# Kernel optimization log

Measured on AMD Instinct MI355X. Metric: run time of the kernel, lower is better.

Reference implementation:

```python
import jax, jax.numpy as jnp
import numpy as np

B, F, C, NS, P, N = 256, 2048, 16384, 65536, 8, 32
T, W_BU, W_H, P_MARGIN, N_MARGIN = 1.0, 1.0, 10.0, 0.1, 0.1


def setup_inputs() -> dict:
    key = jax.random.key(0)
    ks = jax.random.split(key, 8)
    inputs = jax.random.normal(ks[0], (B, F), jnp.float32)
    targets = jax.random.randint(ks[1], (B,), 0, C)
    # batch global indices: unique (original .item() assumes a single match)
    indexs = jax.random.permutation(ks[2], NS)[:B].astype(jnp.int64) if False else jax.random.permutation(ks[2], jnp.arange(NS))[:B]
    # positive candidates drawn from in-batch indices so they are found in `indexs`
    pos_sel = jax.random.randint(ks[3], (B, P), 0, B)
    ppairs = indexs[pos_sel]
    # negative candidates: arbitrary global indices (mostly not in batch)
    npairs = jax.random.randint(ks[4], (B, N), 0, NS)
    all_label_to_clusterid = jax.random.randint(ks[5], (NS,), 0, C)
    V = jax.random.normal(ks[6], (C, F), jnp.float32)
    V = V / jnp.linalg.norm(V, axis=1, keepdims=True)  # bank rows are L2-normalized by the update rule
    return {"inputs": inputs, "targets": targets, "ppairs": ppairs, "npairs": npairs,
            "indexs": indexs, "all_label_to_clusterid": all_label_to_clusterid, "V": V, "epoch": 1}


def _forward(inputs, targets, ppairs, npairs, indexs, all_label_to_clusterid, V, epoch):
    # Exclusive branch: logits against the memory bank (V treated as constant)
    outputs = (inputs @ V.T) * T  # [B, C]
    logp = jax.nn.log_softmax(outputs, axis=1)
    bu_loss = -jnp.mean(jnp.take_along_axis(logp, targets[:, None], axis=1))

    # ms_loss (use_prior=True, use_table=True)
    ni = inputs / jnp.linalg.norm(inputs, axis=1, keepdims=True)
    sims = ni @ ni.T          # [B, B]
    tsims = ni @ V.T          # [B, C]

    # positives found in the batch: (ppair == indexs).nonzero()
    mp = ppairs[:, :, None] == indexs[None, None, :]        # [B, P, B]
    found_p = jnp.any(mp, axis=2)
    idx_p = jnp.argmax(mp, axis=2)
    psim_b = jnp.take_along_axis(sims, idx_p, axis=1)       # [B, P]
    mask_pb = found_p & (ppairs >= 0)
    # table positive: tsims[i, target] appended if nonzero
    tp = jnp.take_along_axis(tsims, targets[:, None], axis=1)  # [B, 1]
    mask_tp = tp != 0
    psims = jnp.concatenate([psim_b, tp], axis=1)           # [B, P+1]
    pmask = jnp.concatenate([mask_pb, mask_tp], axis=1)

    # negatives found in the batch
    mn = npairs[:, :, None] == indexs[None, None, :]        # [B, N, B]
    found_n = jnp.any(mn, axis=2)
    idx_n = jnp.argmax(mn, axis=2)
    nsim_b = jnp.take_along_axis(sims, idx_n, axis=1)       # [B, N]
    mask_nb = found_n & (npairs >= 0)
    # table negative appended for EVERY npair (indent level in original): tsims[i, clusterid[npair]]
    ncid = all_label_to_clusterid[jnp.clip(npairs, 0, None)]
    tn = jnp.take_along_axis(tsims, ncid, axis=1)           # [B, N]
    mask_tn = (npairs >= 0) & (tn != 0)
    nsims = jnp.concatenate([nsim_b, tn], axis=1)           # [B, 2N]
    nmask = jnp.concatenate([mask_nb, mask_tn], axis=1)

    # thresholds: max(nsims) or -3 (+p_margin); min(psims) or 3 (-n_margin)
    p_thrd = jnp.where(jnp.any(nmask, 1), jnp.max(jnp.where(nmask, nsims, -jnp.inf), 1), -3.0) + P_MARGIN
    n_thrd = jnp.where(jnp.any(pmask, 1), jnp.min(jnp.where(pmask, psims, jnp.inf), 1), 3.0) - N_MARGIN

    hp = pmask & (psims < p_thrd[:, None])
    hn = nmask & (nsims > n_thrd[:, None]) & (nsims < 0.999999)

    hp_sum = jnp.sum(jnp.where(hp, jnp.exp(-2.0 * (psims - 0.5)), 0.0))
    hn_sum = jnp.sum(jnp.where(hn, jnp.exp(50.0 * (nsims - 0.5)), 0.0))
    hp_loss = jnp.where(jnp.any(hp), 0.5 * jnp.log1p(hp_sum), 0.0)
    hn_loss = jnp.where(jnp.any(hn), (1.0 / 50.0) * jnp.log1p(hn_sum), 0.0)
    # original builds hpsims/hnsims with torch.tensor(...), which DETACHES them
    h_loss = jax.lax.stop_gradient(hp_loss + hn_loss)

    loss = W_BU * bu_loss + W_H * h_loss
    return loss, outputs


def reference(inputs, targets, ppairs, npairs, indexs, all_label_to_clusterid, V, epoch):
    return _forward(inputs, targets, ppairs, npairs, indexs, all_label_to_clusterid, V, epoch)
```

## Files before the change

kernel.cpp:

```cpp
#include <hip/hip_runtime.h>
#include <hip/hip_bf16.h>
#include <math.h>

#define B_SZ 256
#define F_SZ 2048
#define C_SZ 16384
#define P_SZ 8
#define N_SZ 32

typedef __bf16 bf16x8 __attribute__((ext_vector_type(8)));
typedef float f32x4 __attribute__((ext_vector_type(4)));
typedef unsigned short us8 __attribute__((ext_vector_type(8)));

typedef __attribute__((address_space(3))) unsigned int lds_u32;
typedef __attribute__((address_space(1))) const unsigned int glb_u32;

__device__ __forceinline__ unsigned short f2bf(float x) {
    union { float f; unsigned int u; } v; v.f = x;
    unsigned int r = v.u + 0x7FFFu + ((v.u >> 16) & 1u);
    return (unsigned short)(r >> 16);
}

__global__ __launch_bounds__(256) void prep_kernel(const float* __restrict__ inputs,
                                                   unsigned short* __restrict__ Abf,
                                                   float* __restrict__ norms) {
    const int row = blockIdx.x;
    const int tid = threadIdx.x;
    const float* rp = inputs + (size_t)row * F_SZ + tid * 8;
    float4 v0 = *(const float4*)(rp);
    float4 v1 = *(const float4*)(rp + 4);
    us8 o;
    o[0]=f2bf(v0.x); o[1]=f2bf(v0.y); o[2]=f2bf(v0.z); o[3]=f2bf(v0.w);
    o[4]=f2bf(v1.x); o[5]=f2bf(v1.y); o[6]=f2bf(v1.z); o[7]=f2bf(v1.w);
    *(us8*)(Abf + (size_t)row * F_SZ + tid * 8) = o;
    float ss = v0.x*v0.x + v0.y*v0.y + v0.z*v0.z + v0.w*v0.w
             + v1.x*v1.x + v1.y*v1.y + v1.z*v1.z + v1.w*v1.w;
    __shared__ float red[256];
    red[tid] = ss; __syncthreads();
    for (int s = 128; s > 0; s >>= 1) { if (tid < s) red[tid] += red[tid+s]; __syncthreads(); }
    if (tid == 0) norms[row] = sqrtf(red[0]);
}

#define BM 128
#define BN 64
#define BK 64
#define BPAD 72
#define KITERS (F_SZ / BK)

__global__ __launch_bounds__(256) void gemm_kernel(const unsigned short* __restrict__ Abf,
                                                   const float* __restrict__ V,
                                                   float* __restrict__ Cout) {
    __shared__ unsigned short As[2][BM * BK];
    __shared__ unsigned short Bs[2][BN * BPAD];

    const int tid = threadIdx.x;
    const int lane = tid & 63;
    const int wid = tid >> 6;
    const int q = lane >> 4, l16 = lane & 15;
    const int bm0 = blockIdx.y * BM;
    const int bn0 = blockIdx.x * BN;

    f32x4 acc[2][4];
    #pragma unroll
    for (int i = 0; i < 2; i++)
        #pragma unroll
        for (int j = 0; j < 4; j++) acc[i][j] = (f32x4){0.f, 0.f, 0.f, 0.f};

    const int arow = tid >> 3;
    const int cfetch = (tid & 7) ^ (arow & 7);
    const unsigned short* AgBase = Abf + (size_t)(bm0 + arow) * F_SZ + cfetch * 8;

    const int brow = tid >> 2, bseg = tid & 3;
    const float* BgBase = V + (size_t)(bn0 + brow) * F_SZ + bseg * 16;
    unsigned short* Bsd0 = &Bs[0][brow * BPAD + bseg * 16];
    unsigned short* Bsd1 = &Bs[1][brow * BPAD + bseg * 16];

    float4 b0, b1, b2, b3;

    auto issueA = [&](int buf, int k0) {
        #pragma unroll
        for (int j = 0; j < 4; j++) {
            __builtin_amdgcn_global_load_lds(
                (glb_u32*)(AgBase + (size_t)j * 32 * F_SZ + k0),
                (lds_u32*)&As[buf][(size_t)(j * 256 + wid * 64) * 8],
                16, 0, 0);
        }
    };
    auto loadB = [&](int k0) {
        b0 = *(const float4*)(BgBase + k0);
        b1 = *(const float4*)(BgBase + k0 + 4);
        b2 = *(const float4*)(BgBase + k0 + 8);
        b3 = *(const float4*)(BgBase + k0 + 12);
    };
    auto writeB = [&](unsigned short* dst) {
        us8 w0, w1;
        w0[0]=f2bf(b0.x); w0[1]=f2bf(b0.y); w0[2]=f2bf(b0.z); w0[3]=f2bf(b0.w);
        w0[4]=f2bf(b1.x); w0[5]=f2bf(b1.y); w0[6]=f2bf(b1.z); w0[7]=f2bf(b1.w);
        w1[0]=f2bf(b2.x); w1[1]=f2bf(b2.y); w1[2]=f2bf(b2.z); w1[3]=f2bf(b2.w);
        w1[4]=f2bf(b3.x); w1[5]=f2bf(b3.y); w1[6]=f2bf(b3.z); w1[7]=f2bf(b3.w);
        *(us8*)dst = w0;
        *(us8*)(dst + 8) = w1;
    };

    issueA(0, 0);
    loadB(0);
    writeB(Bsd0);
    __syncthreads();

    for (int it = 0; it < KITERS; ++it) {
        const int cur = it & 1;
        const bool more = (it + 1) < KITERS;
        if (more) {
            issueA(cur ^ 1, (it + 1) * BK);
            loadB((it + 1) * BK);
        }
        #pragma unroll
        for (int ks = 0; ks < 2; ++ks) {
            bf16x8 af[2], bfv[4];
            #pragma unroll
            for (int mi = 0; mi < 2; ++mi) {
                const int row = wid * 32 + mi * 16 + l16;
                const int kc = ks * 4 + q;
                af[mi] = *(const bf16x8*)&As[cur][(size_t)(row * 8 + (kc ^ (row & 7))) * 8];
            }
            #pragma unroll
            for (int ni = 0; ni < 4; ++ni)
                bfv[ni] = *(const bf16x8*)&Bs[cur][(ni * 16 + l16) * BPAD + ks * 32 + q * 8];
            #pragma unroll
            for (int mi = 0; mi < 2; ++mi)
                #pragma unroll
                for (int ni = 0; ni < 4; ++ni)
                    acc[mi][ni] = __builtin_amdgcn_mfma_f32_16x16x32_bf16(af[mi], bfv[ni], acc[mi][ni], 0, 0, 0);
        }
        if (more) writeB(cur ? Bsd0 : Bsd1);
        __syncthreads();
    }

    #pragma unroll
    for (int mi = 0; mi < 2; ++mi) {
        const int r0 = bm0 + wid * 32 + mi * 16 + q * 4;
        #pragma unroll
        for (int ni = 0; ni < 4; ++ni) {
            const int c0 = bn0 + ni * 16 + l16;
            #pragma unroll
            for (int r = 0; r < 4; ++r)
                Cout[(size_t)(r0 + r) * C_SZ + c0] = acc[mi][ni][r];
        }
    }
}

__global__ __launch_bounds__(256) void loss_rows_kernel(
    const float* __restrict__ inputs, const int* __restrict__ targets,
    const int* __restrict__ ppairs, const int* __restrict__ npairs,
    const int* __restrict__ indexs, const int* __restrict__ cluster,
    const float* __restrict__ outputs, const float* __restrict__ norms,
    float* __restrict__ bu_part, float* __restrict__ hp_part,
    float* __restrict__ hn_part, int* __restrict__ flag_part)
{
    const int i = blockIdx.x;
    const int tid = threadIdx.x;
    __shared__ int idxbuf[B_SZ];
    __shared__ int pj[P_SZ];
    __shared__ int nj[N_SZ];
    __shared__ float simp[P_SZ];
    __shared__ float simn[N_SZ];
    __shared__ float tnv[N_SZ];
    __shared__ float red_m[256], red_s[256];
    __shared__ float s_tp;

    idxbuf[tid] = indexs[tid];
    __syncthreads();

    const float* row = outputs + (size_t)i * C_SZ;
    const float ni_norm = norms[i];

    float m = -INFINITY, se = 0.f;
    for (int c = tid; c < C_SZ; c += 256) {
        float v = row[c];
        float nm = fmaxf(m, v);
        se = se * __expf(m - nm) + __expf(v - nm);
        m = nm;
    }
    red_m[tid] = m; red_s[tid] = se; __syncthreads();
    for (int s = 128; s > 0; s >>= 1) {
        if (tid < s) {
            float m2 = red_m[tid + s], s2 = red_s[tid + s];
            float m1 = red_m[tid],      s1 = red_s[tid];
            float nm = fmaxf(m1, m2);
            red_s[tid] = s1 * __expf(m1 - nm) + s2 * __expf(m2 - nm);
            red_m[tid] = nm;
        }
        __syncthreads();
    }

    if (tid < P_SZ) {
        int pp = ppairs[i * P_SZ + tid];
        int f = -1;
        if (pp >= 0) for (int j = 0; j < B_SZ; j++) if (idxbuf[j] == pp) { f = j; break; }
        pj[tid] = f;
    } else if (tid < P_SZ + N_SZ) {
        int t = tid - P_SZ;
        int np = npairs[i * N_SZ + t];
        int f = -1;
        if (np >= 0) for (int j = 0; j < B_SZ; j++) if (idxbuf[j] == np) { f = j; break; }
        nj[t] = f;
        int cid = cluster[np < 0 ? 0 : np];
        tnv[t] = row[cid] / ni_norm;
    }
    if (tid == P_SZ + N_SZ) s_tp = row[targets[i]] / ni_norm;
    __syncthreads();

    const int lane = tid & 63, wv = tid >> 6;
    for (int qq = wv; qq < P_SZ + N_SZ; qq += 4) {
        int j = (qq < P_SZ) ? pj[qq] : nj[qq - P_SZ];
        float s = 0.f;
        if (j >= 0) {
            const float* xi = inputs + (size_t)i * F_SZ;
            const float* xj = inputs + (size_t)j * F_SZ;
            float d = 0.f;
            for (int k = lane; k < F_SZ; k += 64) d += xi[k] * xj[k];
            for (int off = 32; off > 0; off >>= 1) d += __shfl_down(d, off);
            s = d / (ni_norm * norms[j]);
        }
        if (lane == 0) { if (qq < P_SZ) simp[qq] = s; else simn[qq - P_SZ] = s; }
    }
    __syncthreads();

    if (tid == 0) {
        float logZ = red_m[0] + logf(red_s[0]);
        bu_part[i] = -(row[targets[i]] - logZ);

        float psims[P_SZ + 1]; bool pmask[P_SZ + 1];
        for (int p = 0; p < P_SZ; p++) {
            int pp = ppairs[i * P_SZ + p];
            pmask[p] = (pj[p] >= 0) && (pp >= 0);
            psims[p] = simp[p];
        }
        psims[P_SZ] = s_tp; pmask[P_SZ] = (s_tp != 0.0f);

        float nsims[2 * N_SZ]; bool nmask[2 * N_SZ];
        for (int t = 0; t < N_SZ; t++) {
            int np = npairs[i * N_SZ + t];
            nmask[t] = (nj[t] >= 0) && (np >= 0);
            nsims[t] = simn[t];
            nsims[N_SZ + t] = tnv[t];
            nmask[N_SZ + t] = (np >= 0) && (tnv[t] != 0.0f);
        }
        bool anyp = false, anyn = false;
        float maxn = -INFINITY, minp = INFINITY;
        for (int t = 0; t < 2 * N_SZ; t++) if (nmask[t]) { anyn = true; maxn = fmaxf(maxn, nsims[t]); }
        for (int p = 0; p < P_SZ + 1; p++) if (pmask[p]) { anyp = true; minp = fminf(minp, psims[p]); }
        float p_thrd = (anyn ? maxn : -3.0f) + 0.1f;
        float n_thrd = (anyp ? minp : 3.0f) - 0.1f;
        float hps = 0.f, hns = 0.f; int fl = 0;
        for (int p = 0; p < P_SZ + 1; p++)
            if (pmask[p] && psims[p] < p_thrd) { fl |= 1; hps += expf(-2.0f * (psims[p] - 0.5f)); }
        for (int t = 0; t < 2 * N_SZ; t++)
            if (nmask[t] && nsims[t] > n_thrd && nsims[t] < 0.999999f) { fl |= 2; hns += expf(50.0f * (nsims[t] - 0.5f)); }
        hp_part[i] = hps; hn_part[i] = hns; flag_part[i] = fl;
    }
}

__global__ __launch_bounds__(256) void finalize_kernel(
    const float* __restrict__ bu_part, const float* __restrict__ hp_part,
    const float* __restrict__ hn_part, const int* __restrict__ flag_part,
    float* __restrict__ d_out)
{
    __shared__ float r1[256], r2[256], r3[256];
    __shared__ int rf[256];
    const int tid = threadIdx.x;
    r1[tid] = bu_part[tid]; r2[tid] = hp_part[tid]; r3[tid] = hn_part[tid]; rf[tid] = flag_part[tid];
    __syncthreads();
    for (int s = 128; s > 0; s >>= 1) {
        if (tid < s) { r1[tid] += r1[tid+s]; r2[tid] += r2[tid+s]; r3[tid] += r3[tid+s]; rf[tid] |= rf[tid+s]; }
        __syncthreads();
    }
    if (tid == 0) {
        float bu = r1[0] / (float)B_SZ;
        float hp_loss = (rf[0] & 1) ? 0.5f * log1pf(r2[0]) : 0.0f;
        float hn_loss = (rf[0] & 2) ? (1.0f / 50.0f) * log1pf(r3[0]) : 0.0f;
        d_out[0] = 1.0f * bu + 10.0f * (hp_loss + hn_loss);
    }
}

extern "C" void kernel_launch(void* const* d_in, const int* in_sizes, int n_in,
                              void* d_out, int out_size, void* d_ws, size_t ws_size,
                              hipStream_t stream) {
    const float* inputs  = (const float*)d_in[0];
    const int*   targets = (const int*)d_in[1];
    const int*   ppairs  = (const int*)d_in[2];
    const int*   npairs  = (const int*)d_in[3];
    const int*   indexs  = (const int*)d_in[4];
    const int*   cluster = (const int*)d_in[5];
    const float* V       = (const float*)d_in[6];
    float* out = (float*)d_out;

    char* ws = (char*)d_ws;
    unsigned short* Abf = (unsigned short*)ws;
    float* norms   = (float*)(ws + (size_t)B_SZ * F_SZ * 2);
    float* bu_part = norms + B_SZ;
    float* hp_part = bu_part + B_SZ;
    float* hn_part = hp_part + B_SZ;
    int*   flag_part = (int*)(hn_part + B_SZ);

    prep_kernel<<<B_SZ, 256, 0, stream>>>(inputs, Abf, norms);
    gemm_kernel<<<dim3(C_SZ / BN, B_SZ / BM), 256, 0, stream>>>(Abf, V, out + 1);
    loss_rows_kernel<<<B_SZ, 256, 0, stream>>>(inputs, targets, ppairs, npairs, indexs,
                                               cluster, out + 1, norms,
                                               bu_part, hp_part, hn_part, flag_part);
    finalize_kernel<<<1, 256, 0, stream>>>(bu_part, hp_part, hn_part, flag_part, out);
}
```

Baseline: 316.9 us.

## Fuse per-tile softmax max/sum into GEMM epilogue and split loss kernel

The GEMM epilogue now computes a per-row, per-column-tile running max and sum of exponentials from the accumulators and writes them to workspace. A new combine kernel merges the 256 partials per row to get logZ and the cross-entropy term. The pair-similarity work moves to a separate kernel, so the 16 MB logits matrix no longer has to be reread for the softmax. The cost is extra shuffles and exps in the GEMM epilogue, one more kernel launch, and 512 KB of partials.

Result: faster. 302.8 us (-4.5%).

```diff
diff --git a/kernel.cpp b/kernel.cpp
--- a/kernel.cpp
+++ b/kernel.cpp
@@ -7,6 +7,7 @@
 #define C_SZ 16384
 #define P_SZ 8
 #define N_SZ 32
+#define NTILE 256
 
 typedef __bf16 bf16x8 __attribute__((ext_vector_type(8)));
 typedef float f32x4 __attribute__((ext_vector_type(4)));
@@ -49,7 +50,9 @@
 
 __global__ __launch_bounds__(256) void gemm_kernel(const unsigned short* __restrict__ Abf,
                                                    const float* __restrict__ V,
-                                                   float* __restrict__ Cout) {
+                                                   float* __restrict__ Cout,
+                                                   float* __restrict__ pmax,
+                                                   float* __restrict__ psum) {
     __shared__ unsigned short As[2][BM * BK];
     __shared__ unsigned short Bs[2][BN * BPAD];
 
@@ -147,15 +150,65 @@
                 Cout[(size_t)(r0 + r) * C_SZ + c0] = acc[mi][ni][r];
         }
     }
-}
-
-__global__ __launch_bounds__(256) void loss_rows_kernel(
+
+    const int tileIdx = blockIdx.x;
+    #pragma unroll
+    for (int mi = 0; mi < 2; ++mi) {
+        #pragma unroll
+        for (int r = 0; r < 4; ++r) {
+            float mloc = fmaxf(fmaxf(acc[mi][0][r], acc[mi][1][r]),
+                               fmaxf(acc[mi][2][r], acc[mi][3][r]));
+            #pragma unroll
+            for (int off = 1; off < 16; off <<= 1)
+                mloc = fmaxf(mloc, __shfl_xor(mloc, off, 64));
+            float sloc = __expf(acc[mi][0][r] - mloc) + __expf(acc[mi][1][r] - mloc)
+                       + __expf(acc[mi][2][r] - mloc) + __expf(acc[mi][3][r] - mloc);
+            #pragma unroll
+            for (int off = 1; off < 16; off <<= 1)
+                sloc += __shfl_xor(sloc, off, 64);
+            if (l16 == 0) {
+                const int grow = bm0 + wid * 32 + mi * 16 + q * 4 + r;
+                pmax[grow * NTILE + tileIdx] = mloc;
+                psum[grow * NTILE + tileIdx] = sloc;
+            }
+        }
+    }
+}
+
+__global__ __launch_bounds__(256) void softmax_combine_kernel(
+    const float* __restrict__ pmax, const float* __restrict__ psum,
+    const float* __restrict__ outputs, const int* __restrict__ targets,
+    float* __restrict__ bu_part)
+{
+    const int row = blockIdx.x;
+    const int tid = threadIdx.x;
+    __shared__ float rm[256], rs[256];
+    rm[tid] = pmax[row * NTILE + tid];
+    rs[tid] = psum[row * NTILE + tid];
+    __syncthreads();
+    for (int s = 128; s > 0; s >>= 1) {
+        if (tid < s) {
+            float m1 = rm[tid], s1 = rs[tid];
+            float m2 = rm[tid + s], s2 = rs[tid + s];
+            float nm = fmaxf(m1, m2);
+            rs[tid] = s1 * __expf(m1 - nm) + s2 * __expf(m2 - nm);
+            rm[tid] = nm;
+        }
+        __syncthreads();
+    }
+    if (tid == 0) {
+        float logZ = rm[0] + logf(rs[0]);
+        bu_part[row] = -(outputs[(size_t)row * C_SZ + targets[row]] - logZ);
+    }
+}
+
+__global__ __launch_bounds__(256) void pairs_kernel(
     const float* __restrict__ inputs, const int* __restrict__ targets,
     const int* __restrict__ ppairs, const int* __restrict__ npairs,
     const int* __restrict__ indexs, const int* __restrict__ cluster,
     const float* __restrict__ outputs, const float* __restrict__ norms,
-    float* __restrict__ bu_part, float* __restrict__ hp_part,
-    float* __restrict__ hn_part, int* __restrict__ flag_part)
+    float* __restrict__ hp_part, float* __restrict__ hn_part,
+    int* __restrict__ flag_part)
 {
     const int i = blockIdx.x;
     const int tid = threadIdx.x;
@@ -165,7 +218,6 @@
     __shared__ float simp[P_SZ];
     __shared__ float simn[N_SZ];
     __shared__ float tnv[N_SZ];
-    __shared__ float red_m[256], red_s[256];
     __shared__ float s_tp;
 
     idxbuf[tid] = indexs[tid];
@@ -173,25 +225,6 @@
 
     const float* row = outputs + (size_t)i * C_SZ;
     const float ni_norm = norms[i];
-
-    float m = -INFINITY, se = 0.f;
-    for (int c = tid; c < C_SZ; c += 256) {
-        float v = row[c];
-        float nm = fmaxf(m, v);
-        se = se * __expf(m - nm) + __expf(v - nm);
-        m = nm;
-    }
-    red_m[tid] = m; red_s[tid] = se; __syncthreads();
-    for (int s = 128; s > 0; s >>= 1) {
-        if (tid < s) {
-            float m2 = red_m[tid + s], s2 = red_s[tid + s];
-            float m1 = red_m[tid],      s1 = red_s[tid];
-            float nm = fmaxf(m1, m2);
-            red_s[tid] = s1 * __expf(m1 - nm) + s2 * __expf(m2 - nm);
-            red_m[tid] = nm;
-        }
-        __syncthreads();
-    }
 
     if (tid < P_SZ) {
         int pp = ppairs[i * P_SZ + tid];
@@ -227,9 +260,6 @@
     __syncthreads();
 
     if (tid == 0) {
-        float logZ = red_m[0] + logf(red_s[0]);
-        bu_part[i] = -(row[targets[i]] - logZ);
-
         float psims[P_SZ + 1]; bool pmask[P_SZ + 1];
         for (int p = 0; p < P_SZ; p++) {
             int pp = ppairs[i * P_SZ + p];
@@ -302,11 +332,14 @@
     float* hp_part = bu_part + B_SZ;
     float* hn_part = hp_part + B_SZ;
     int*   flag_part = (int*)(hn_part + B_SZ);
+    float* pmax = (float*)(flag_part + B_SZ);
+    float* psum = pmax + (size_t)B_SZ * NTILE;
 
     prep_kernel<<<B_SZ, 256, 0, stream>>>(inputs, Abf, norms);
-    gemm_kernel<<<dim3(C_SZ / BN, B_SZ / BM), 256, 0, stream>>>(Abf, V, out + 1);
-    loss_rows_kernel<<<B_SZ, 256, 0, stream>>>(inputs, targets, ppairs, npairs, indexs,
-                                               cluster, out + 1, norms,
-                                               bu_part, hp_part, hn_part, flag_part);
+    gemm_kernel<<<dim3(C_SZ / BN, B_SZ / BM), 256, 0, stream>>>(Abf, V, out + 1, pmax, psum);
+    softmax_combine_kernel<<<B_SZ, 256, 0, stream>>>(pmax, psum, out + 1, targets, bu_part);
+    pairs_kernel<<<B_SZ, 256, 0, stream>>>(inputs, targets, ppairs, npairs, indexs,
+                                           cluster, out + 1, norms,
+                                           hp_part, hn_part, flag_part);
     finalize_kernel<<<1, 256, 0, stream>>>(bu_part, hp_part, hn_part, flag_part, out);
 }
```
